# Kernel optimization log

Measured on AMD Instinct MI355X. Metric: run time of the kernel, lower is better.

## Reference

```python
import jax, jax.numpy as jnp
import numpy as np

S = 1024      # sequence length
V = 32000     # vocab size
H = 1024      # hidden_dim
A = 128       # attn_size (module default)


def lstm_cell(x, h, c, Wih, Whh, b):
    # torch LSTM gate order: i, f, g, o
    g = x @ Wih.T + h @ Whh.T + b
    i, f, gg, o = jnp.split(g, 4)
    c = jax.nn.sigmoid(f) * c + jax.nn.sigmoid(i) * jnp.tanh(gg)
    h = jax.nn.sigmoid(o) * jnp.tanh(c)
    return h, c


def setup_inputs() -> dict:
    key = jax.random.key(0)
    ks = jax.random.split(key, 16)
    p = lambda k, shape: (jax.random.normal(k, shape, jnp.float32) * 0.02)
    return {
        'input_seq': jax.random.randint(ks[0], (S,), 0, V),
        'gold_seq': jax.random.randint(ks[1], (S,), 0, V),
        'embed': p(ks[2], (V, H)),
        'enc_Wih': p(ks[3], (4 * H, H)),
        'enc_Whh': p(ks[4], (4 * H, H)),
        'enc_b': jnp.zeros((4 * H,), jnp.float32),   # b_ih + b_hh combined
        'dec_Wih': p(ks[5], (4 * H, 2 * H)),          # decoder input = [prev, context]
        'dec_Whh': p(ks[6], (4 * H, H)),
        'dec_b': jnp.zeros((4 * H,), jnp.float32),
        'U_w': p(ks[7], (A, H)), 'U_b': jnp.zeros((A,), jnp.float32),
        'Wa_w': p(ks[8], (A, H)), 'Wa_b': jnp.zeros((A,), jnp.float32),
        'Va_w': p(ks[9], (1, A)), 'Va_b': jnp.zeros((1,), jnp.float32),
        'out_w': p(ks[10], (V, H)), 'out_b': jnp.zeros((V,), jnp.float32),
    }


def reference(input_seq, gold_seq, embed, enc_Wih, enc_Whh, enc_b,
              dec_Wih, dec_Whh, dec_b, U_w, U_b, Wa_w, Wa_b, Va_w, Va_b,
              out_w, out_b):
    Hd = embed.shape[1]
    x_emb = embed[input_seq]  # (S, H)

    def enc_step(carry, x):
        h, c = carry
        h, c = lstm_cell(x, h, c, enc_Wih, enc_Whh, enc_b)
        return (h, c), h

    zero = jnp.zeros((Hd,), x_emb.dtype)
    (h0, c0), enc_out = jax.lax.scan(enc_step, (zero, zero), x_emb)  # enc_out: (S, H)

    U_enc = enc_out @ U_w.T + U_b  # (S, A), hidden-independent part of additive attention

    # teacher forcing: prev_0 = zeros, prev_i = embed(gold[i-1]); relu applied each step
    prev = jnp.concatenate([jnp.zeros((1, Hd), x_emb.dtype), embed[gold_seq[:-1]]], axis=0)
    prev = jax.nn.relu(prev)  # (S, H)

    def dec_step(carry, p):
        h, c = carry
        # additive attention scores: V(tanh(U(enc) + W(h)))  -> (S, 1)
        scores = jnp.tanh(U_enc + h @ Wa_w.T + Wa_b) @ Va_w.T + Va_b
        # faithful to nn.Softmax() on a (S,1) tensor: torch picks dim=1 -> all ones
        w = jax.nn.softmax(scores, axis=1)  # (S, 1), == ones
        context = w[:, 0] @ enc_out         # (H,) == sum of encoder outputs
        x = jnp.concatenate([p, context])   # (2H,)
        h, c = lstm_cell(x, h, c, dec_Wih, dec_Whh, dec_b)
        logits = h @ out_w.T + out_b        # (V,)
        return (h, c), (logits, jnp.argmax(logits))

    _, (preds, idxs) = jax.lax.scan(dec_step, (h0, c0), prev)
    return preds, idxs  # (S, V) float logits, (S,) predicted ids
```

## Files before the change

### kernel.cpp

```cpp
#include <hip/hip_runtime.h>
#include <math.h>


#define S_LEN 1024
#define HDIM  1024
#define VDIM  32000

typedef float f4 __attribute__((ext_vector_type(4)));
typedef float f32x4 __attribute__((ext_vector_type(4)));
typedef short short8 __attribute__((ext_vector_type(8)));
typedef short sh4 __attribute__((ext_vector_type(4)));

__device__ __forceinline__ void agent_storef(float* p, float v) {
    __hip_atomic_store(p, v, __ATOMIC_RELAXED, __HIP_MEMORY_SCOPE_AGENT);
}
__device__ __forceinline__ float sigmoidf_(float x) {
    return 1.0f / (1.0f + expf(-x));
}
__device__ __forceinline__ void llc_load_4x4(const float* p, f4& a, f4& b,
                                             f4& c, f4& d) {
    asm volatile(
        "global_load_dwordx4 %0, %4, off sc0 sc1\n\t"
        "global_load_dwordx4 %1, %4, off offset:1024 sc0 sc1\n\t"
        "global_load_dwordx4 %2, %4, off offset:2048 sc0 sc1\n\t"
        "global_load_dwordx4 %3, %4, off offset:3072 sc0 sc1\n\t"
        "s_waitcnt vmcnt(0)"
        : "=&v"(a), "=&v"(b), "=&v"(c), "=&v"(d)
        : "v"(p) : "memory");
}
__device__ __forceinline__ bool any_nan16(f4 a, f4 b, f4 c, f4 d) {
    float s0 = (a.x + a.y) + (a.z + a.w);
    float s1 = (b.x + b.y) + (b.z + b.w);
    float s2 = (c.x + c.y) + (c.z + c.w);
    float s3 = (d.x + d.y) + (d.z + d.w);
    float s  = (s0 + s1) + (s2 + s3);
    return s != s;
}
__device__ __forceinline__ int swz(int s) {
    return (s & ~7) | ((s ^ (s >> 3)) & 7);
}
__device__ __forceinline__ void split_bf16(float x, unsigned short& h,
                                           unsigned short& l) {
    unsigned u = __float_as_uint(x);
    unsigned hr = (u + 0x7FFFu + ((u >> 16) & 1u)) >> 16;
    h = (unsigned short)hr;
    float hf = __uint_as_float(hr << 16);
    float r = x - hf;
    unsigned v = __float_as_uint(r);
    l = (unsigned short)((v + 0x7FFFu + ((v >> 16) & 1u)) >> 16);
}

#define LSTR 40

template<int MODE>
__global__ __launch_bounds__(512, 1)
void g_mfma(const float* __restrict__ B, int ldb,
            const float* __restrict__ bias,
            float* __restrict__ C, int ldc,
            const float* __restrict__ embed,
            const int* __restrict__ gidx)
{
    __shared__ unsigned short Ah[256][LSTR], Al[256][LSTR];
    __shared__ unsigned short Bh[128][LSTR], Bl[128][LSTR];

    const int tid = threadIdx.x;
    const int l   = tid & 63;
    const int w   = tid >> 6;
    const int n0  = blockIdx.x * 128;
    const int m0  = blockIdx.y * 256;
    const int mb  = (w >> 1) * 64;
    const int nb  = (w & 1) * 64;

    int  arow[4];
    bool azero[4];
#pragma unroll
    for (int q = 0; q < 4; ++q) {
        int row = (q * 512 + tid) >> 3;
        int m = m0 + row;
        if (MODE == 1) { arow[q] = gidx[m]; azero[q] = false; }
        else { azero[q] = (m == 0); arow[q] = azero[q] ? 0 : gidx[m - 1]; }
    }

    f32x4 acc[4][4];
#pragma unroll
    for (int i = 0; i < 4; ++i)
#pragma unroll
        for (int jj = 0; jj < 4; ++jj) acc[i][jj] = (f32x4){0.f, 0.f, 0.f, 0.f};

    for (int k0 = 0; k0 < HDIM; k0 += 32) {
#pragma unroll
        for (int q = 0; q < 4; ++q) {
            int id  = q * 512 + tid;
            int row = id >> 3;
            int kq  = (id & 7) * 4;
            float4 av;
            if (MODE == 2 && azero[q]) {
                av = make_float4(0.f, 0.f, 0.f, 0.f);
            } else {
                av = *(const float4*)(embed + (size_t)arow[q] * HDIM + k0 + kq);
                if (MODE == 2) {
                    av.x = fmaxf(av.x, 0.f); av.y = fmaxf(av.y, 0.f);
                    av.z = fmaxf(av.z, 0.f); av.w = fmaxf(av.w, 0.f);
                }
            }
            unsigned short h0,h1,h2,h3, l0,l1,l2,l3;
            split_bf16(av.x, h0, l0); split_bf16(av.y, h1, l1);
            split_bf16(av.z, h2, l2); split_bf16(av.w, h3, l3);
            sh4 hi = {(short)h0, (short)h1, (short)h2, (short)h3};
            sh4 lo = {(short)l0, (short)l1, (short)l2, (short)l3};
            *(sh4*)&Ah[row][kq] = hi;
            *(sh4*)&Al[row][kq] = lo;
        }
#pragma unroll
        for (int q = 0; q < 2; ++q) {
            int id  = q * 512 + tid;
            int row = id >> 3;
            int kq  = (id & 7) * 4;
            float4 bv = *(const float4*)(B + (size_t)(n0 + row) * ldb
                                         + k0 + kq);
            unsigned short h0,h1,h2,h3, l0,l1,l2,l3;
            split_bf16(bv.x, h0, l0); split_bf16(bv.y, h1, l1);
            split_bf16(bv.z, h2, l2); split_bf16(bv.w, h3, l3);
            sh4 hi = {(short)h0, (short)h1, (short)h2, (short)h3};
            sh4 lo = {(short)l0, (short)l1, (short)l2, (short)l3};
            *(sh4*)&Bh[row][kq] = hi;
            *(sh4*)&Bl[row][kq] = lo;
        }
        __syncthreads();

        const int kb = (l >> 4) * 8;
        short8 a_hi[4], a_lo[4], b_hi[4], b_lo[4];
#pragma unroll
        for (int i = 0; i < 4; ++i) {
            int ra = mb + i * 16 + (l & 15);
            int rb = nb + i * 16 + (l & 15);
            a_hi[i] = *(const short8*)&Ah[ra][kb];
            a_lo[i] = *(const short8*)&Al[ra][kb];
            b_hi[i] = *(const short8*)&Bh[rb][kb];
            b_lo[i] = *(const short8*)&Bl[rb][kb];
        }
#pragma unroll
        for (int i = 0; i < 4; ++i)
#pragma unroll
            for (int jj = 0; jj < 4; ++jj) {
                acc[i][jj] = __builtin_amdgcn_mfma_f32_16x16x32_bf16(
                    a_hi[i], b_hi[jj], acc[i][jj], 0, 0, 0);
                acc[i][jj] = __builtin_amdgcn_mfma_f32_16x16x32_bf16(
                    a_hi[i], b_lo[jj], acc[i][jj], 0, 0, 0);
                acc[i][jj] = __builtin_amdgcn_mfma_f32_16x16x32_bf16(
                    a_lo[i], b_hi[jj], acc[i][jj], 0, 0, 0);
            }
        __syncthreads();
    }

#pragma unroll
    for (int i = 0; i < 4; ++i) {
        const int mrow = m0 + mb + i * 16 + ((l >> 4) << 2);
#pragma unroll
        for (int jj = 0; jj < 4; ++jj) {
            int n = n0 + nb + jj * 16 + (l & 15);
            float bv = bias[n];
            f32x4 o = acc[i][jj];
#pragma unroll
            for (int r = 0; r < 4; ++r)
                C[(size_t)(mrow + r) * ldc + n] = o[r] + bv;
        }
    }
}

__global__ __launch_bounds__(512, 2)
void lstm_seq(const float* __restrict__ Whh,
              const float* __restrict__ G,
              const float* __restrict__ h_init,
              const float* __restrict__ c_init,
              float* __restrict__ h_out,
              float* __restrict__ c_fin,
              float* __restrict__ csum_out,
              int slen)
{
    __shared__ f4 hbuf[2][256];
    const int tid = threadIdx.x;
    const int g   = blockIdx.x;
    const int wv  = tid >> 6;
    const int lg  = tid & 63;
    const int j   = g * 8 + wv;

    f4 W[4][4];
#pragma unroll
    for (int q = 0; q < 4; ++q)
#pragma unroll
        for (int i = 0; i < 4; ++i)
            W[q][i] = *(const f4*)(Whh + (size_t)(j + q * HDIM) * HDIM
                                   + 4 * lg + 256 * i);

    float c = 0.0f, csum = 0.0f;
    if (lg == 0) c = c_init[j];

    float gnow = G[(size_t)(lg & 3) * HDIM + j];

    for (int t = 0; t < slen; ++t) {
#pragma unroll
        for (int q = 0; q < 4; ++q)
#pragma unroll
            for (int i = 0; i < 4; ++i)
                asm volatile("" : "+v"(W[q][i]));

        const float* hp = (t == 0) ? h_init : (h_out + (size_t)(t - 1) * HDIM);
        f4* hb = hbuf[t & 1];

        if (wv == 0) {
            f4 a, b, cc, d;
            const float* p = hp + 4 * lg;
            for (;;) {
                llc_load_4x4(p, a, b, cc, d);
                if (!__any(any_nan16(a, b, cc, d))) break;
                __builtin_amdgcn_s_sleep(1);
            }
            hb[swz(lg)]       = a;
            hb[swz(64 + lg)]  = b;
            hb[swz(128 + lg)] = cc;
            hb[swz(192 + lg)] = d;
        }
        __syncthreads();

        int tn = (t + 1 < slen) ? (t + 1) : t;
        float gnext = G[(size_t)tn * (4 * HDIM) + (lg & 3) * HDIM + j];

        f4 h0 = hb[swz(lg)];
        f4 h1 = hb[swz(64 + lg)];
        f4 h2 = hb[swz(128 + lg)];
        f4 h3 = hb[swz(192 + lg)];
        float p0 = 0.f, p1 = 0.f, p2 = 0.f, p3 = 0.f;
        f4 hv;
#pragma unroll
        for (int i = 0; i < 4; ++i) {
            hv = (i == 0) ? h0 : (i == 1) ? h1 : (i == 2) ? h2 : h3;
            p0 = fmaf(W[0][i].x, hv.x, fmaf(W[0][i].y, hv.y,
                 fmaf(W[0][i].z, hv.z, fmaf(W[0][i].w, hv.w, p0))));
            p1 = fmaf(W[1][i].x, hv.x, fmaf(W[1][i].y, hv.y,
                 fmaf(W[1][i].z, hv.z, fmaf(W[1][i].w, hv.w, p1))));
            p2 = fmaf(W[2][i].x, hv.x, fmaf(W[2][i].y, hv.y,
                 fmaf(W[2][i].z, hv.z, fmaf(W[2][i].w, hv.w, p2))));
            p3 = fmaf(W[3][i].x, hv.x, fmaf(W[3][i].y, hv.y,
                 fmaf(W[3][i].z, hv.z, fmaf(W[3][i].w, hv.w, p3))));
        }

        float t01 = __shfl_xor((lg & 1) ? p0 : p1, 1);
        float s01 = ((lg & 1) ? p1 : p0) + t01;
        float t23 = __shfl_xor((lg & 1) ? p2 : p3, 1);
        float s23 = ((lg & 1) ? p3 : p2) + t23;
        float tq  = __shfl_xor((lg & 2) ? s01 : s23, 2);
        float s   = ((lg & 2) ? s23 : s01) + tq;
        s += __shfl_xor(s, 4);
        s += __shfl_xor(s, 8);
        s += __shfl_xor(s, 16);
        s += __shfl_xor(s, 32);

        float pre = s + gnow;
        float act = ((lg & 3) == 2) ? tanhf(pre) : sigmoidf_(pre);
        float a1 = __shfl(act, 1);
        float a2 = __shfl(act, 2);
        float a3 = __shfl(act, 3);

        if (lg == 0) {
            c = a1 * c + act * a2;
            float h = a3 * tanhf(c);
            csum += h;
            agent_storef(h_out + (size_t)t * HDIM + j, h);
        }
        gnow = gnext;
    }

    if (lg == 0) {
        if (c_fin)    c_fin[j]    = c;
        if (csum_out) csum_out[j] = csum;
    }
}

__global__ __launch_bounds__(256)
void ctx_bias_k(const float* __restrict__ dec_Wih,
                const float* __restrict__ dec_b,
                const float* __restrict__ ctx,
                float* __restrict__ out)
{
    const int wv = threadIdx.x >> 6;
    const int lane = threadIdx.x & 63;
    const int r = blockIdx.x * 4 + wv;
    const float* wr = dec_Wih + (size_t)r * (2 * HDIM) + HDIM;
    float s = 0.f;
    for (int k = lane; k < HDIM; k += 64) s += wr[k] * ctx[k];
#pragma unroll
    for (int off = 32; off > 0; off >>= 1) s += __shfl_xor(s, off);
    if (lane == 0) out[r] = s + dec_b[r];
}

__global__ __launch_bounds__(512, 1)
void logits_mfma(const float* __restrict__ Amat,
                 const float* __restrict__ Bmat,
                 const float* __restrict__ bias,
                 float* __restrict__ C,
                 unsigned long long* __restrict__ amax)
{
    __shared__ unsigned short Ah[256][LSTR], Al[256][LSTR];
    __shared__ unsigned short Bh[128][LSTR], Bl[128][LSTR];

    const int tid = threadIdx.x;
    const int l   = tid & 63;
    const int w   = tid >> 6;
    const int n0  = blockIdx.x * 128;
    const int m0  = blockIdx.y * 256;
    const int mb  = (w >> 1) * 64;
    const int nb  = (w & 1) * 64;

    f32x4 acc[4][4];
#pragma unroll
    for (int i = 0; i < 4; ++i)
#pragma unroll
        for (int jj = 0; jj < 4; ++jj) acc[i][jj] = (f32x4){0.f, 0.f, 0.f, 0.f};

    for (int k0 = 0; k0 < HDIM; k0 += 32) {
#pragma unroll
        for (int q = 0; q < 4; ++q) {
            int id  = q * 512 + tid;
            int row = id >> 3;
            int kq  = (id & 7) * 4;
            float4 av = *(const float4*)(Amat + (size_t)(m0 + row) * HDIM
                                         + k0 + kq);
            unsigned short h0,h1,h2,h3, l0,l1,l2,l3;
            split_bf16(av.x, h0, l0); split_bf16(av.y, h1, l1);
            split_bf16(av.z, h2, l2); split_bf16(av.w, h3, l3);
            sh4 hi = {(short)h0, (short)h1, (short)h2, (short)h3};
            sh4 lo = {(short)l0, (short)l1, (short)l2, (short)l3};
            *(sh4*)&Ah[row][kq] = hi;
            *(sh4*)&Al[row][kq] = lo;
        }
#pragma unroll
        for (int q = 0; q < 2; ++q) {
            int id  = q * 512 + tid;
            int row = id >> 3;
            int kq  = (id & 7) * 4;
            float4 bv = *(const float4*)(Bmat + (size_t)(n0 + row) * HDIM
                                         + k0 + kq);
            unsigned short h0,h1,h2,h3, l0,l1,l2,l3;
            split_bf16(bv.x, h0, l0); split_bf16(bv.y, h1, l1);
            split_bf16(bv.z, h2, l2); split_bf16(bv.w, h3, l3);
            sh4 hi = {(short)h0, (short)h1, (short)h2, (short)h3};
            sh4 lo = {(short)l0, (short)l1, (short)l2, (short)l3};
            *(sh4*)&Bh[row][kq] = hi;
            *(sh4*)&Bl[row][kq] = lo;
        }
        __syncthreads();

        const int kb = (l >> 4) * 8;
        short8 a_hi[4], a_lo[4], b_hi[4], b_lo[4];
#pragma unroll
        for (int i = 0; i < 4; ++i) {
            int ra = mb + i * 16 + (l & 15);
            int rb = nb + i * 16 + (l & 15);
            a_hi[i] = *(const short8*)&Ah[ra][kb];
            a_lo[i] = *(const short8*)&Al[ra][kb];
            b_hi[i] = *(const short8*)&Bh[rb][kb];
            b_lo[i] = *(const short8*)&Bl[rb][kb];
        }
#pragma unroll
        for (int i = 0; i < 4; ++i)
#pragma unroll
            for (int jj = 0; jj < 4; ++jj) {
                acc[i][jj] = __builtin_amdgcn_mfma_f32_16x16x32_bf16(
                    a_hi[i], b_hi[jj], acc[i][jj], 0, 0, 0);
                acc[i][jj] = __builtin_amdgcn_mfma_f32_16x16x32_bf16(
                    a_hi[i], b_lo[jj], acc[i][jj], 0, 0, 0);
                acc[i][jj] = __builtin_amdgcn_mfma_f32_16x16x32_bf16(
                    a_lo[i], b_hi[jj], acc[i][jj], 0, 0, 0);
            }
        __syncthreads();
    }

#pragma unroll
    for (int i = 0; i < 4; ++i) {
        const int mrow = m0 + mb + i * 16 + ((l >> 4) << 2);
        unsigned long long key[4] = {0ull, 0ull, 0ull, 0ull};
#pragma unroll
        for (int jj = 0; jj < 4; ++jj) {
            int n = n0 + nb + jj * 16 + (l & 15);
            float bv = bias[n];
            f32x4 o = acc[i][jj];
#pragma unroll
            for (int r = 0; r < 4; ++r) {
                float val = o[r] + bv;
                C[(size_t)(mrow + r) * VDIM + n] = val;
                unsigned um = __float_as_uint(val);
                um = (um & 0x80000000u) ? ~um : (um | 0x80000000u);
                unsigned long long k2 = ((unsigned long long)um << 32)
                    | (unsigned long long)(0xFFFFFFFFu - (unsigned)n);
                if (k2 > key[r]) key[r] = k2;
            }
        }
#pragma unroll
        for (int r = 0; r < 4; ++r) {
#pragma unroll
            for (int off = 1; off < 16; off <<= 1) {
                unsigned long long other = __shfl_xor(key[r], off);
                if (other > key[r]) key[r] = other;
            }
            if ((l & 15) == 0)
                atomicMax(&amax[mrow + r], key[r]);
        }
    }
}

__global__ __launch_bounds__(256)
void idx_final(const unsigned long long* __restrict__ amax,
               float* __restrict__ out_idx)
{
    int i = blockIdx.x * 256 + threadIdx.x;
    if (i < S_LEN) {
        unsigned col = 0xFFFFFFFFu - (unsigned)(amax[i] & 0xFFFFFFFFull);
        out_idx[i] = (float)col;
    }
}

extern "C" void kernel_launch(void* const* d_in, const int* in_sizes, int n_in,
                              void* d_out, int out_size, void* d_ws, size_t ws_size,
                              hipStream_t stream)
{
    (void)in_sizes; (void)n_in; (void)out_size; (void)ws_size;

    const int*   input_seq = (const int*)d_in[0];
    const int*   gold_seq  = (const int*)d_in[1];
    const float* embed     = (const float*)d_in[2];
    const float* enc_Wih   = (const float*)d_in[3];
    const float* enc_Whh   = (const float*)d_in[4];
    const float* enc_b     = (const float*)d_in[5];
    const float* dec_Wih   = (const float*)d_in[6];
    const float* dec_Whh   = (const float*)d_in[7];
    const float* dec_b     = (const float*)d_in[8];
    const float* out_w     = (const float*)d_in[15];
    const float* out_b     = (const float*)d_in[16];

    float* out = (float*)d_out;
    float* G_enc = out;
    float* G_dec = out + 4194304;

    char* wsb = (char*)d_ws;
    unsigned long long* amax = (unsigned long long*)wsb;
    float* zerovec = (float*)(wsb + 8192);
    float* c0      = zerovec + 1024;
    float* ctx     = c0 + 1024;
    float* ctxb    = ctx + 1024;
    float* enc_out = ctxb + 4096;
    float* dec_h   = enc_out + 1048576;

    hipMemsetAsync(d_ws, 0, 12288, stream);
    hipMemsetAsync(enc_out, 0xFF, (size_t)S_LEN * HDIM * 4, stream);
    hipMemsetAsync(dec_h,   0xFF, (size_t)S_LEN * HDIM * 4, stream);

    g_mfma<1><<<dim3(32, 4), 512, 0, stream>>>(
        enc_Wih, HDIM, enc_b, G_enc, 4 * HDIM, embed, input_seq);

    lstm_seq<<<128, 512, 0, stream>>>(
        enc_Whh, G_enc, zerovec, zerovec, enc_out, c0, ctx, S_LEN);

    ctx_bias_k<<<1024, 256, 0, stream>>>(dec_Wih, dec_b, ctx, ctxb);

    g_mfma<2><<<dim3(32, 4), 512, 0, stream>>>(
        dec_Wih, 2 * HDIM, ctxb, G_dec, 4 * HDIM, embed, gold_seq);

    lstm_seq<<<128, 512, 0, stream>>>(
        dec_Whh, G_dec, enc_out + (size_t)(S_LEN - 1) * HDIM, c0,
        dec_h, nullptr, nullptr, S_LEN);

    logits_mfma<<<dim3(VDIM / 128, S_LEN / 256), 512, 0, stream>>>(
        dec_h, out_w, out_b, out, amax);

    idx_final<<<4, 256, 0, stream>>>(amax, out + (size_t)S_LEN * VDIM);
}
```

Measured before the change: 4.372 ms.

## Merge encoder and decoder input-gate GEMMs into one launch; reorder logits grid

Runs the encoder and decoder input-projection GEMMs together in a single 256-block launch, since the decoder projection of the previous-token embeddings does not depend on the encoder. The context-dependent bias is then added afterwards by a small elementwise kernel. This fills more of the GPU in one launch and takes the decoder GEMM off the serial path after the encoder LSTM, at the cost of an extra read-modify-write pass over G_dec. The logits grid is also transposed so consecutive blocks share the same out_w tile across M blocks, which should improve L2 reuse.

```diff
diff --git a/kernel.cpp b/kernel.cpp
--- a/kernel.cpp
+++ b/kernel.cpp
@@ -53,12 +53,12 @@
 #define LSTR 40
 
 template<int MODE>
-__global__ __launch_bounds__(512, 1)
-void g_mfma(const float* __restrict__ B, int ldb,
-            const float* __restrict__ bias,
-            float* __restrict__ C, int ldc,
-            const float* __restrict__ embed,
-            const int* __restrict__ gidx)
+__device__ void g_body(const float* __restrict__ B, int ldb,
+                       const float* __restrict__ bias,
+                       float* __restrict__ C, int ldc,
+                       const float* __restrict__ embed,
+                       const int* __restrict__ gidx,
+                       int bx, int byy)
 {
     __shared__ unsigned short Ah[256][LSTR], Al[256][LSTR];
     __shared__ unsigned short Bh[128][LSTR], Bl[128][LSTR];
@@ -66,8 +66,8 @@
     const int tid = threadIdx.x;
     const int l   = tid & 63;
     const int w   = tid >> 6;
-    const int n0  = blockIdx.x * 128;
-    const int m0  = blockIdx.y * 256;
+    const int n0  = bx * 128;
+    const int m0  = byy * 256;
     const int mb  = (w >> 1) * 64;
     const int nb  = (w & 1) * 64;
 
@@ -159,12 +159,46 @@
 #pragma unroll
         for (int jj = 0; jj < 4; ++jj) {
             int n = n0 + nb + jj * 16 + (l & 15);
-            float bv = bias[n];
+            float bv = bias ? bias[n] : 0.f;
             f32x4 o = acc[i][jj];
 #pragma unroll
             for (int r = 0; r < 4; ++r)
                 C[(size_t)(mrow + r) * ldc + n] = o[r] + bv;
         }
+    }
+}
+
+__global__ __launch_bounds__(512, 1)
+void g_mfma_both(const float* __restrict__ embed,
+                 const int* __restrict__ input_seq,
+                 const int* __restrict__ gold_seq,
+                 const float* __restrict__ enc_Wih,
+                 const float* __restrict__ enc_b,
+                 const float* __restrict__ dec_Wih,
+                 float* __restrict__ G_enc,
+                 float* __restrict__ G_dec)
+{
+    const int by = blockIdx.y;
+    if (by < 4)
+        g_body<1>(enc_Wih, HDIM, enc_b, G_enc, 4 * HDIM,
+                  embed, input_seq, blockIdx.x, by);
+    else
+        g_body<2>(dec_Wih, 2 * HDIM, nullptr, G_dec, 4 * HDIM,
+                  embed, gold_seq, blockIdx.x, by - 4);
+}
+
+__global__ __launch_bounds__(256)
+void gdec_add(float* __restrict__ G, const float* __restrict__ ctxb)
+{
+    const int row = blockIdx.x;
+    float* gp = G + (size_t)row * (4 * HDIM);
+#pragma unroll
+    for (int q = 0; q < 4; ++q) {
+        int idx = (q * 256 + threadIdx.x) * 4;
+        f4 v = *(f4*)(gp + idx);
+        f4 b = *(const f4*)(ctxb + idx);
+        v.x += b.x; v.y += b.y; v.z += b.z; v.w += b.w;
+        *(f4*)(gp + idx) = v;
     }
 }
 
@@ -307,8 +341,8 @@
     const int tid = threadIdx.x;
     const int l   = tid & 63;
     const int w   = tid >> 6;
-    const int n0  = blockIdx.x * 128;
-    const int m0  = blockIdx.y * 256;
+    const int n0  = blockIdx.y * 128;
+    const int m0  = blockIdx.x * 256;
     const int mb  = (w >> 1) * 64;
     const int nb  = (w & 1) * 64;
 
@@ -455,22 +489,21 @@
     hipMemsetAsync(enc_out, 0xFF, (size_t)S_LEN * HDIM * 4, stream);
     hipMemsetAsync(dec_h,   0xFF, (size_t)S_LEN * HDIM * 4, stream);
 
-    g_mfma<1><<<dim3(32, 4), 512, 0, stream>>>(
-        enc_Wih, HDIM, enc_b, G_enc, 4 * HDIM, embed, input_seq);
+    g_mfma_both<<<dim3(32, 8), 512, 0, stream>>>(
+        embed, input_seq, gold_seq, enc_Wih, enc_b, dec_Wih, G_enc, G_dec);
 
     lstm_seq<<<128, 512, 0, stream>>>(
         enc_Whh, G_enc, zerovec, zerovec, enc_out, c0, ctx, S_LEN);
 
     ctx_bias_k<<<1024, 256, 0, stream>>>(dec_Wih, dec_b, ctx, ctxb);
 
-    g_mfma<2><<<dim3(32, 4), 512, 0, stream>>>(
-        dec_Wih, 2 * HDIM, ctxb, G_dec, 4 * HDIM, embed, gold_seq);
+    gdec_add<<<1024, 256, 0, stream>>>(G_dec, ctxb);
 
     lstm_seq<<<128, 512, 0, stream>>>(
         dec_Whh, G_dec, enc_out + (size_t)(S_LEN - 1) * HDIM, c0,
         dec_h, nullptr, nullptr, S_LEN);
 
-    logits_mfma<<<dim3(VDIM / 128, S_LEN / 256), 512, 0, stream>>>(
+    logits_mfma<<<dim3(S_LEN / 256, VDIM / 128), 512, 0, stream>>>(
         dec_h, out_w, out_b, out, amax);
 
     idx_final<<<4, 256, 0, stream>>>(amax, out + (size_t)S_LEN * VDIM);
```

Result: no change. 4.324 ms (-1.1%).
